# Kernel tuning notes

Measured on AMD Instinct MI355X. Metric: run time of the kernel, lower is better.

## Reference

```python
import jax, jax.numpy as jnp
import numpy as np

N_NODES = 100000


def _gcn_conv(x, W, b, src, dst, n):
    # PyG GCNConv (default): add self-loops, norm = deg^{-1/2}[src] * deg^{-1/2}[dst]
    # degree computed on target nodes (col) with unit edge weights, then
    # out[i] = sum_{(j->i)} norm_ji * (x_j @ W) + b
    loops = jnp.arange(n, dtype=src.dtype)
    s = jnp.concatenate([src, loops])
    d = jnp.concatenate([dst, loops])
    deg = jax.ops.segment_sum(jnp.ones_like(d, dtype=x.dtype), d, num_segments=n)
    dinv = jnp.where(deg > 0, jax.lax.rsqrt(deg), 0.0)
    h = x @ W                                  # [n, out_dim]
    norm = (dinv[s] * dinv[d])[:, None]        # [E+n, 1]
    msg = h[s] * norm                          # gather + scale
    out = jax.ops.segment_sum(msg, d, num_segments=n)  # scatter-add to targets
    return out + b


def setup_inputs() -> dict:
    key = jax.random.key(0)
    ks = jax.random.split(key, 4)
    x = jax.random.normal(ks[0], (N_NODES, 128), dtype=jnp.float32)
    edge_index = jax.random.randint(ks[1], (2, 1600000), 0, N_NODES, dtype=jnp.int64)
    W1 = jax.random.normal(ks[2], (128, 16), dtype=jnp.float32) * (1.0 / np.sqrt(128))
    b1 = jnp.zeros((16,), dtype=jnp.float32)
    W2 = jax.random.normal(ks[3], (16, 3), dtype=jnp.float32) * (1.0 / np.sqrt(16))
    b2 = jnp.zeros((3,), dtype=jnp.float32)
    return {"x": x, "edge_index": edge_index, "W1": W1, "b1": b1, "W2": W2, "b2": b2}


def reference(x, edge_index, W1, b1, W2, b2):
    src, dst = edge_index[0], edge_index[1]
    n = x.shape[0]
    h = _gcn_conv(x, W1, b1, src, dst, n)
    h = jax.nn.relu(h)
    # F.dropout in eval mode == identity (deterministic baseline)
    h = _gcn_conv(h, W2, b2, src, dst, n)
    return jax.nn.log_softmax(h, axis=1)
```

## Files before the change

### kernel.cpp

```cpp
#include <hip/hip_runtime.h>
#include <hip/hip_fp16.h>
#include <math.h>


#define BSH 9
#define BNODES 512
#define P1 512
#define GROWS 64

struct alignas(8) Half4 { __half x, y, z, w; };

__global__ void k1a_count(const int* __restrict__ dst, int* __restrict__ hist_t,
                          int NBK, int E) {
    __shared__ int lh[256];
    int t = threadIdx.x;
    lh[t] = 0;
    __syncthreads();
    int slice = (E + P1 - 1) / P1;
    int e0 = blockIdx.x * slice, e1 = min(E, e0 + slice);
    for (int e = e0 + t; e < e1; e += 256)
        atomicAdd(&lh[dst[e] >> BSH], 1);
    __syncthreads();
    for (int i = t; i < NBK; i += 256)
        hist_t[(size_t)i * P1 + blockIdx.x] = lh[i];
}

__global__ void kscan1(const int* __restrict__ hist_t, int* __restrict__ colpre_t,
                       int* __restrict__ btot, int NBK) {
    __shared__ int v[P1], part[256];
    int kb = blockIdx.x, t = threadIdx.x;
    v[t] = hist_t[(size_t)kb * P1 + t];
    v[t + 256] = hist_t[(size_t)kb * P1 + t + 256];
    __syncthreads();
    int a = v[2 * t], c = v[2 * t + 1];
    part[t] = a + c;
    __syncthreads();
    for (int o = 1; o < 256; o <<= 1) {
        int add = (t >= o) ? part[t - o] : 0;
        __syncthreads();
        part[t] += add;
        __syncthreads();
    }
    int pre = (t == 0) ? 0 : part[t - 1];
    colpre_t[(size_t)kb * P1 + 2 * t] = pre;
    colpre_t[(size_t)kb * P1 + 2 * t + 1] = pre + a;
    if (t == 255) btot[kb] = part[255];
}

__global__ void kscan2(const int* __restrict__ btot, int* __restrict__ bucket_base, int NBK) {
    __shared__ int s[256];
    int t = threadIdx.x;
    int orig = (t < NBK) ? btot[t] : 0;
    s[t] = orig;
    __syncthreads();
    for (int o = 1; o < 256; o <<= 1) {
        int add = (t >= o) ? s[t - o] : 0;
        __syncthreads();
        s[t] += add;
        __syncthreads();
    }
    if (t < NBK) {
        bucket_base[t] = s[t] - orig;
        if (t == NBK - 1) bucket_base[NBK] = s[t];
    }
}

__global__ void k1b_fat(const int* __restrict__ src, const int* __restrict__ dst,
                        const int* __restrict__ colpre_t, const int* __restrict__ bucket_base,
                        unsigned int* __restrict__ staging,
                        const float* __restrict__ x, const float* __restrict__ W1,
                        Half4* __restrict__ g1h, int NBK, int n, int E) {
    __shared__ float sx[GROWS * 132];
    __shared__ float4 sW4[512];
    int b = blockIdx.x;
    if (b < P1) {
        int* loff = (int*)sx;
        int* lcur = ((int*)sx) + 1024;
        for (int i = threadIdx.x; i < NBK; i += 256) {
            loff[i] = bucket_base[i] + colpre_t[(size_t)i * P1 + b];
            lcur[i] = 0;
        }
        __syncthreads();
        int slice = (E + P1 - 1) / P1;
        int e0 = b * slice, e1 = min(E, e0 + slice);
        for (int e = e0 + threadIdx.x; e < e1; e += 256) {
            int d = dst[e], s = src[e];
            int k = d >> BSH;
            int t = atomicAdd(&lcur[k], 1);
            staging[loff[k] + t] = ((unsigned int)s << BSH) | (unsigned int)(d & (BNODES - 1));
        }
    } else {
        int t = threadIdx.x;
        int base = (b - P1) * GROWS;
        for (int i = t; i < 512; i += 256) sW4[i] = ((const float4*)W1)[i];
        for (int i = t; i < GROWS * 32; i += 256) {
            int r = i >> 5, c = i & 31;
            int row = base + r;
            float4 v = (row < n) ? ((const float4*)x)[(size_t)row * 32 + c]
                                 : make_float4(0.f, 0.f, 0.f, 0.f);
            *((float4*)&sx[r * 132 + c * 4]) = v;
        }
        __syncthreads();
        int r = t >> 2, c4 = t & 3;
        int row = base + r;
        if (row >= n) return;
        float4 acc = make_float4(0.f, 0.f, 0.f, 0.f);
        #pragma unroll 8
        for (int q = 0; q < 32; ++q) {
            float4 xv = *((const float4*)&sx[r * 132 + q * 4]);
            #pragma unroll
            for (int j = 0; j < 4; ++j) {
                float s = (j == 0) ? xv.x : (j == 1) ? xv.y : (j == 2) ? xv.z : xv.w;
                float4 w = sW4[(q * 4 + j) * 4 + c4];
                acc.x += s * w.x; acc.y += s * w.y; acc.z += s * w.z; acc.w += s * w.w;
            }
        }
        Half4 h;
        h.x = __float2half(acc.x); h.y = __float2half(acc.y);
        h.z = __float2half(acc.z); h.w = __float2half(acc.w);
        g1h[(size_t)row * 4 + c4] = h;
    }
}

__global__ void __launch_bounds__(1024) k2_bucket(
        const unsigned int* __restrict__ staging, const int* __restrict__ bucket_base,
        int* __restrict__ csr, int* __restrict__ deg, float* __restrict__ dinv,
        int* __restrict__ row_start, Half4* __restrict__ g1h, int n) {
    __shared__ int lh[BNODES], sc[BNODES], lcur[BNODES];
    __shared__ float ldv[BNODES];
    int kb = blockIdx.x, t = threadIdx.x;
    int node0 = kb << BSH;
    int nloc = min(BNODES, n - node0);
    int ebase = bucket_base[kb], ecnt = bucket_base[kb + 1] - ebase;
    if (t < BNODES) { lh[t] = 0; lcur[t] = 0; }
    __syncthreads();
    for (int e = t; e < ecnt; e += 1024)
        atomicAdd(&lh[staging[ebase + e] & (BNODES - 1)], 1);
    __syncthreads();
    int own = 0;
    if (t < BNODES) { own = lh[t]; sc[t] = own; }
    __syncthreads();
    for (int o = 1; o < BNODES; o <<= 1) {
        int add = 0;
        if (t < BNODES && t >= o) add = sc[t - o];
        __syncthreads();
        if (t < BNODES) sc[t] += add;
        __syncthreads();
    }
    if (t < BNODES) {
        int excl = sc[t] - own;
        if (t < nloc) {
            deg[node0 + t] = own;
            row_start[node0 + t] = ebase + excl;
            float dv = rsqrtf((float)(own + 1));
            dinv[node0 + t] = dv;
            ldv[t] = dv;
        }
        sc[t] = excl;
    }
    __syncthreads();
    for (int e = t; e < ecnt; e += 1024) {
        unsigned int p = staging[ebase + e];
        int loc = p & (BNODES - 1);
        int s = (int)(p >> BSH);
        int tk = atomicAdd(&lcur[loc], 1);
        csr[ebase + sc[loc] + tk] = s;
    }
    for (int j = t; j < nloc * 4; j += 1024) {
        float dv = ldv[j >> 2];
        Half4 v = g1h[(size_t)node0 * 4 + j];
        v.x = __float2half(__half2float(v.x) * dv);
        v.y = __float2half(__half2float(v.y) * dv);
        v.z = __float2half(__half2float(v.z) * dv);
        v.w = __float2half(__half2float(v.w) * dv);
        g1h[(size_t)node0 * 4 + j] = v;
    }
}

__global__ void k_gather1(const uint4* __restrict__ g1q, const int* __restrict__ csr,
                          const int* __restrict__ row_start, const int* __restrict__ deg,
                          const float* __restrict__ dinv, const float* __restrict__ b1,
                          const float* __restrict__ W2, Half4* __restrict__ g2h, int n) {
    int idx = blockIdx.x * 256 + threadIdx.x;
    int i = idx >> 4, l = idx & 15;
    if (i >= n) return;
    int off = row_start[i], dg = deg[i];
    float acc[16];
    #pragma unroll
    for (int j = 0; j < 16; ++j) acc[j] = 0.f;
    if (l == 0) {
        uint4 p0 = g1q[2 * (size_t)i], p1 = g1q[2 * (size_t)i + 1];
        const __half2* h0 = reinterpret_cast<const __half2*>(&p0);
        const __half2* h1 = reinterpret_cast<const __half2*>(&p1);
        #pragma unroll
        for (int j = 0; j < 4; ++j) {
            float2 f0 = __half22float2(h0[j]);
            float2 f1 = __half22float2(h1[j]);
            acc[2 * j] += f0.x; acc[2 * j + 1] += f0.y;
            acc[8 + 2 * j] += f1.x; acc[9 + 2 * j] += f1.y;
        }
    }
    for (int k = l; k < dg; k += 16) {
        int s = csr[off + k];
        uint4 p0 = g1q[2 * (size_t)s], p1 = g1q[2 * (size_t)s + 1];
        const __half2* h0 = reinterpret_cast<const __half2*>(&p0);
        const __half2* h1 = reinterpret_cast<const __half2*>(&p1);
        #pragma unroll
        for (int j = 0; j < 4; ++j) {
            float2 f0 = __half22float2(h0[j]);
            float2 f1 = __half22float2(h1[j]);
            acc[2 * j] += f0.x; acc[2 * j + 1] += f0.y;
            acc[8 + 2 * j] += f1.x; acc[9 + 2 * j] += f1.y;
        }
    }
    #pragma unroll
    for (int m = 1; m < 16; m <<= 1) {
        #pragma unroll
        for (int j = 0; j < 16; ++j) acc[j] += __shfl_xor(acc[j], m);
    }
    if (l != 0) return;
    float di = dinv[i];
    float o0 = 0.f, o1 = 0.f, o2 = 0.f;
    #pragma unroll
    for (int c = 0; c < 16; ++c) {
        float z = fmaxf(0.f, di * acc[c] + b1[c]);
        o0 += z * W2[c * 3 + 0];
        o1 += z * W2[c * 3 + 1];
        o2 += z * W2[c * 3 + 2];
    }
    Half4 g;
    g.x = __float2half(di * o0); g.y = __float2half(di * o1);
    g.z = __float2half(di * o2); g.w = __float2half(0.f);
    g2h[i] = g;
}

__global__ void k_gather2(const Half4* __restrict__ g2h, const int* __restrict__ csr,
                          const int* __restrict__ row_start, const int* __restrict__ deg,
                          const float* __restrict__ dinv, const float* __restrict__ b2,
                          float* __restrict__ out, int n) {
    int idx = blockIdx.x * 256 + threadIdx.x;
    int i = idx >> 4, l = idx & 15;
    if (i >= n) return;
    int off = row_start[i], dg = deg[i];
    float v0 = 0.f, v1 = 0.f, v2 = 0.f;
    if (l == 0) {
        Half4 s = g2h[i];
        v0 = __half2float(s.x); v1 = __half2float(s.y); v2 = __half2float(s.z);
    }
    for (int e = l; e < dg; e += 16) {
        int s = csr[off + e];
        Half4 g = g2h[s];
        v0 += __half2float(g.x); v1 += __half2float(g.y); v2 += __half2float(g.z);
    }
    #pragma unroll
    for (int o = 1; o < 16; o <<= 1) {
        v0 += __shfl_xor(v0, o);
        v1 += __shfl_xor(v1, o);
        v2 += __shfl_xor(v2, o);
    }
    if (l >= 3) return;
    float di = dinv[i];
    float a0 = di * v0 + b2[0];
    float a1 = di * v1 + b2[1];
    float a2 = di * v2 + b2[2];
    float m = fmaxf(a0, fmaxf(a1, a2));
    float lse = logf(expf(a0 - m) + expf(a1 - m) + expf(a2 - m));
    float r = (l == 0) ? a0 : (l == 1) ? a1 : a2;
    out[(size_t)i * 3 + l] = r - m - lse;
}

extern "C" void kernel_launch(void* const* d_in, const int* in_sizes, int n_in,
                              void* d_out, int out_size, void* d_ws, size_t ws_size,
                              hipStream_t stream) {
    const float* x  = (const float*)d_in[0];
    const int*   ei = (const int*)d_in[1];
    const float* W1 = (const float*)d_in[2];
    const float* b1 = (const float*)d_in[3];
    const float* W2 = (const float*)d_in[4];
    const float* b2 = (const float*)d_in[5];
    float* out = (float*)d_out;

    const int n = in_sizes[0] / 128;
    const int E = in_sizes[1] / 2;
    const int* src = ei;
    const int* dst = ei + E;

    const int NBK = (n + BNODES - 1) >> BSH;

    auto align = [](size_t v) { return (v + 255) & ~(size_t)255; };
    char* ws = (char*)d_ws;
    size_t o = 0;
    int* hist_t      = (int*)(ws + o); o = align(o + (size_t)NBK * P1 * 4);
    int* colpre_t    = (int*)(ws + o); o = align(o + (size_t)NBK * P1 * 4);
    int* btot        = (int*)(ws + o); o = align(o + (size_t)NBK * 4);
    int* bucket_base = (int*)(ws + o); o = align(o + (size_t)(NBK + 1) * 4);
    int* deg         = (int*)(ws + o); o = align(o + (size_t)n * 4);
    float* dinv      = (float*)(ws + o); o = align(o + (size_t)n * 4);
    int* row_start   = (int*)(ws + o); o = align(o + (size_t)n * 4);
    unsigned int* staging = (unsigned int*)(ws + o); o = align(o + (size_t)E * 4);
    int* csr         = (int*)(ws + o); o = align(o + (size_t)E * 4);
    Half4* g1h       = (Half4*)(ws + o); o = align(o + (size_t)n * 4 * 8);
    Half4* g2h       = (Half4*)(ws + o); o = align(o + (size_t)n * 8);

    const int B = 256;
    int gGemm = (n + GROWS - 1) / GROWS;
    int gn16  = (16 * n + B - 1) / B;

    k1a_count<<<P1, B, 0, stream>>>(dst, hist_t, NBK, E);
    kscan1<<<NBK, B, 0, stream>>>(hist_t, colpre_t, btot, NBK);
    kscan2<<<1, B, 0, stream>>>(btot, bucket_base, NBK);
    k1b_fat<<<P1 + gGemm, B, 0, stream>>>(src, dst, colpre_t, bucket_base, staging,
                                          x, W1, g1h, NBK, n, E);
    k2_bucket<<<NBK, 1024, 0, stream>>>(staging, bucket_base, csr, deg, dinv, row_start,
                                        g1h, n);
    k_gather1<<<gn16, B, 0, stream>>>((const uint4*)g1h, csr, row_start, deg, dinv, b1, W2,
                                      g2h, n);
    k_gather2<<<gn16, B, 0, stream>>>(g2h, csr, row_start, deg, dinv, b2, out, n);
}
```

Before: 182.0 us.

## Stage bucket scatters in shared memory for coalesced staging and CSR writes

The partition kernel now builds a per-block local histogram and prefix scan, writes edges sorted by bucket into a shared-memory buffer along with their global addresses, and then writes staging out in a second pass that is contiguous within each bucket. The bucket kernel likewise assembles its CSR segment in a shared buffer (when the edge count fits) and writes it out contiguously. The aim is to replace scattered global writes with mostly coalesced ones. The cost is an extra pass over dst, more shared memory and syncs, and lower occupancy from the larger LDS footprint.

```diff
diff --git a/kernel.cpp b/kernel.cpp
--- a/kernel.cpp
+++ b/kernel.cpp
@@ -7,6 +7,7 @@
 #define BNODES 512
 #define P1 512
 #define GROWS 64
+#define K2BUF 10240
 
 struct alignas(8) Half4 { __half x, y, z, w; };
 
@@ -74,21 +75,47 @@
     __shared__ float4 sW4[512];
     int b = blockIdx.x;
     if (b < P1) {
-        int* loff = (int*)sx;
-        int* lcur = ((int*)sx) + 1024;
-        for (int i = threadIdx.x; i < NBK; i += 256) {
+        int* hist  = (int*)sx;
+        int* cs    = hist + 256;
+        int* loff  = hist + 512;
+        int* cur   = hist + 768;
+        int* buf   = hist + 1024;
+        int* gaddr = buf + 3200;
+        int t = threadIdx.x;
+        hist[t] = 0; cur[t] = 0;
+        for (int i = t; i < NBK; i += 256)
             loff[i] = bucket_base[i] + colpre_t[(size_t)i * P1 + b];
-            lcur[i] = 0;
-        }
         __syncthreads();
         int slice = (E + P1 - 1) / P1;
         int e0 = b * slice, e1 = min(E, e0 + slice);
-        for (int e = e0 + threadIdx.x; e < e1; e += 256) {
+        int len = e1 - e0;
+        for (int e = e0 + t; e < e1; e += 256)
+            atomicAdd(&hist[dst[e] >> BSH], 1);
+        __syncthreads();
+        int h = hist[t];
+        cs[t] = h;
+        __syncthreads();
+        for (int o = 1; o < 256; o <<= 1) {
+            int add = (t >= o) ? cs[t - o] : 0;
+            __syncthreads();
+            cs[t] += add;
+            __syncthreads();
+        }
+        int incl = cs[t];
+        __syncthreads();
+        cs[t] = incl - h;
+        __syncthreads();
+        for (int e = e0 + t; e < e1; e += 256) {
             int d = dst[e], s = src[e];
             int k = d >> BSH;
-            int t = atomicAdd(&lcur[k], 1);
-            staging[loff[k] + t] = ((unsigned int)s << BSH) | (unsigned int)(d & (BNODES - 1));
-        }
+            int tk = atomicAdd(&cur[k], 1);
+            int pos = cs[k] + tk;
+            buf[pos] = (s << BSH) | (d & (BNODES - 1));
+            gaddr[pos] = loff[k] + tk;
+        }
+        __syncthreads();
+        for (int p = t; p < len; p += 256)
+            staging[gaddr[p]] = (unsigned int)buf[p];
     } else {
         int t = threadIdx.x;
         int base = (b - P1) * GROWS;
@@ -115,10 +142,10 @@
                 acc.x += s * w.x; acc.y += s * w.y; acc.z += s * w.z; acc.w += s * w.w;
             }
         }
-        Half4 h;
-        h.x = __float2half(acc.x); h.y = __float2half(acc.y);
-        h.z = __float2half(acc.z); h.w = __float2half(acc.w);
-        g1h[(size_t)row * 4 + c4] = h;
+        Half4 hh;
+        hh.x = __float2half(acc.x); hh.y = __float2half(acc.y);
+        hh.z = __float2half(acc.z); hh.w = __float2half(acc.w);
+        g1h[(size_t)row * 4 + c4] = hh;
     }
 }
 
@@ -128,6 +155,7 @@
         int* __restrict__ row_start, Half4* __restrict__ g1h, int n) {
     __shared__ int lh[BNODES], sc[BNODES], lcur[BNODES];
     __shared__ float ldv[BNODES];
+    __shared__ int buf[K2BUF];
     int kb = blockIdx.x, t = threadIdx.x;
     int node0 = kb << BSH;
     int nloc = min(BNODES, n - node0);
@@ -159,12 +187,23 @@
         sc[t] = excl;
     }
     __syncthreads();
-    for (int e = t; e < ecnt; e += 1024) {
-        unsigned int p = staging[ebase + e];
-        int loc = p & (BNODES - 1);
-        int s = (int)(p >> BSH);
-        int tk = atomicAdd(&lcur[loc], 1);
-        csr[ebase + sc[loc] + tk] = s;
+    if (ecnt <= K2BUF) {
+        for (int e = t; e < ecnt; e += 1024) {
+            unsigned int p = staging[ebase + e];
+            int loc = p & (BNODES - 1);
+            int tk = atomicAdd(&lcur[loc], 1);
+            buf[sc[loc] + tk] = (int)(p >> BSH);
+        }
+        __syncthreads();
+        for (int p = t; p < ecnt; p += 1024)
+            csr[ebase + p] = buf[p];
+    } else {
+        for (int e = t; e < ecnt; e += 1024) {
+            unsigned int p = staging[ebase + e];
+            int loc = p & (BNODES - 1);
+            int tk = atomicAdd(&lcur[loc], 1);
+            csr[ebase + sc[loc] + tk] = (int)(p >> BSH);
+        }
     }
     for (int j = t; j < nloc * 4; j += 1024) {
         float dv = ldv[j >> 2];
```

After: 171.2 us. 5.9% less time.
